# Optimization experiments

Measured on AMD Instinct MI355X. Metric: run time of the kernel, lower is better.

Reference implementation:

```python
import jax, jax.numpy as jnp
import numpy as np

B, T, C, H = 2, 2048, 2048, 16
HS = C // H
EPS = 1e-5


def _ln(x, w, b):
    mu = jnp.mean(x, axis=-1, keepdims=True)
    var = jnp.mean(jnp.square(x - mu), axis=-1, keepdims=True)
    return (x - mu) * jax.lax.rsqrt(var + EPS) * w + b


def setup_inputs() -> dict:
    key = jax.random.key(0)
    ks = jax.random.split(key, 8)
    s = 0.02
    return {
        "x": jax.random.normal(ks[0], (B, T, C), jnp.float32),
        "ln1_w": jnp.ones((C,), jnp.float32),
        "ln1_b": jnp.zeros((C,), jnp.float32),
        "w_qkv": jax.random.normal(ks[1], (C, 3 * C), jnp.float32) * s,
        "b_qkv": jnp.zeros((3 * C,), jnp.float32),
        "w_proj": jax.random.normal(ks[2], (C, C), jnp.float32) * s,
        "b_proj": jnp.zeros((C,), jnp.float32),
        "ln2_w": jnp.ones((C,), jnp.float32),
        "ln2_b": jnp.zeros((C,), jnp.float32),
        "w_fc": jax.random.normal(ks[3], (C, 4 * C), jnp.float32) * s,
        "b_fc": jnp.zeros((4 * C,), jnp.float32),
        "w_fc2": jax.random.normal(ks[4], (4 * C, C), jnp.float32) * s,
        "b_fc2": jnp.zeros((C,), jnp.float32),
    }


def reference(x, ln1_w, ln1_b, w_qkv, b_qkv, w_proj, b_proj,
              ln2_w, ln2_b, w_fc, b_fc, w_fc2, b_fc2):
    # --- attention branch (kv_cache=None -> L=0, burst=False, no padding mask) ---
    h = _ln(x, ln1_w, ln1_b)
    qkv = h @ w_qkv + b_qkv  # (B, T, 3C)
    q, k, v = jnp.split(qkv, 3, axis=-1)
    q = q.reshape(B, T, H, HS).transpose(0, 2, 1, 3)  # (B, H, T, HS)
    k = k.reshape(B, T, H, HS).transpose(0, 2, 1, 3)
    v = v.reshape(B, T, H, HS).transpose(0, 2, 1, 3)
    att = jnp.einsum('bhqd,bhkd->bhqk', q, k) * (1.0 / np.sqrt(HS))
    causal = jnp.tril(jnp.ones((T, T), bool))  # bias[0:T, 0:T]
    att = jnp.where(causal, att, -jnp.inf)
    att = jax.nn.softmax(att, axis=-1)
    y = jnp.einsum('bhqk,bhkd->bhqd', att, v)
    y = y.transpose(0, 2, 1, 3).reshape(B, T, C)
    y = y @ w_proj + b_proj
    x = x + y
    # --- MLP branch ---
    h = _ln(x, ln2_w, ln2_b)
    h = jax.nn.gelu(h @ w_fc + b_fc, approximate=False)
    x = x + (h @ w_fc2 + b_fc2)
    return x
```

## Files before the change

kernel.cpp:

```cpp
#include <hip/hip_runtime.h>
#include <hip/hip_bf16.h>
#include <cstdint>
#include <cstddef>

typedef __attribute__((ext_vector_type(8))) short bf16x8;
typedef __attribute__((ext_vector_type(4))) float f32x4;

#define DEVI __device__ __forceinline__

DEVI unsigned short f2bf(float f) {
  union { float f; unsigned u; } x; x.f = f;
  unsigned r = x.u + 0x7fffu + ((x.u >> 16) & 1u);
  return (unsigned short)(r >> 16);
}

DEVI float exp2fast(float x) {
#if __has_builtin(__builtin_amdgcn_exp2f)
  return __builtin_amdgcn_exp2f(x);
#else
  return exp2f(x);
#endif
}

DEVI void gload_lds16(const void* g, void* l) {
  __builtin_amdgcn_global_load_lds((const __attribute__((address_space(1))) void*)g,
                                   (__attribute__((address_space(3))) void*)l, 16, 0, 0);
}

DEVI f32x4 mfma16(bf16x8 a, bf16x8 b, f32x4 c) {
  return __builtin_amdgcn_mfma_f32_16x16x32_bf16(a, b, c, 0, 0, 0);
}

__global__ __launch_bounds__(256) void transpose_to_bf16(
    const float* __restrict__ w, unsigned short* __restrict__ wt, int K, int N) {
  __shared__ float tile[32][33];
  const int n0 = blockIdx.x * 32, k0 = blockIdx.y * 32;
  const int tx = threadIdx.x, ty = threadIdx.y;
#pragma unroll
  for (int i = 0; i < 4; i++)
    tile[ty + i * 8][tx] = w[(size_t)(k0 + ty + i * 8) * N + n0 + tx];
  __syncthreads();
#pragma unroll
  for (int i = 0; i < 4; i++)
    wt[(size_t)(n0 + ty + i * 8) * K + k0 + tx] = f2bf(tile[tx][ty + i * 8]);
}

__global__ __launch_bounds__(256) void transpose_v(
    const unsigned short* __restrict__ in, unsigned short* __restrict__ out) {
  __shared__ unsigned short tile[32][33];
  const int bh = blockIdx.z;
  const unsigned short* inp = in + (size_t)bh * 2048 * 128;
  unsigned short* op = out + (size_t)bh * 2048 * 128;
  const int t0 = blockIdx.x * 32, d0 = blockIdx.y * 32;
  const int tx = threadIdx.x, ty = threadIdx.y;
#pragma unroll
  for (int i = 0; i < 4; i++)
    tile[ty + i * 8][tx] = inp[(size_t)(t0 + ty + i * 8) * 128 + d0 + tx];
  __syncthreads();
#pragma unroll
  for (int i = 0; i < 4; i++)
    op[(size_t)(d0 + ty + i * 8) * 2048 + t0 + tx] = tile[tx][ty + i * 8];
}

__global__ __launch_bounds__(256) void ln_kernel(
    const float* __restrict__ x, const float* __restrict__ gw,
    const float* __restrict__ gb, unsigned short* __restrict__ out) {
  __shared__ float red[8];
  const int row = blockIdx.x, tid = threadIdx.x;
  const float* xr = x + (size_t)row * 2048;
  f32x4 a = *((const f32x4*)xr + tid * 2);
  f32x4 b = *((const f32x4*)xr + tid * 2 + 1);
  float s = a[0] + a[1] + a[2] + a[3] + b[0] + b[1] + b[2] + b[3];
#pragma unroll
  for (int m = 32; m >= 1; m >>= 1) s += __shfl_xor(s, m, 64);
  if ((tid & 63) == 0) red[tid >> 6] = s;
  __syncthreads();
  const float mu = (red[0] + red[1] + red[2] + red[3]) * (1.f / 2048.f);
  float d[8]; float ss = 0.f;
#pragma unroll
  for (int j = 0; j < 8; j++) {
    float v = ((j < 4) ? a[j] : b[j - 4]) - mu;
    d[j] = v; ss += v * v;
  }
#pragma unroll
  for (int m = 32; m >= 1; m >>= 1) ss += __shfl_xor(ss, m, 64);
  __syncthreads();
  if ((tid & 63) == 0) red[4 + (tid >> 6)] = ss;
  __syncthreads();
  const float var = (red[4] + red[5] + red[6] + red[7]) * (1.f / 2048.f);
  const float rstd = rsqrtf(var + 1e-5f);
  f32x4 w0 = *((const f32x4*)gw + tid * 2), w1 = *((const f32x4*)gw + tid * 2 + 1);
  f32x4 b0 = *((const f32x4*)gb + tid * 2), b1 = *((const f32x4*)gb + tid * 2 + 1);
  union { bf16x8 v; unsigned short u[8]; } o;
#pragma unroll
  for (int j = 0; j < 8; j++) {
    float wv = (j < 4) ? w0[j] : w1[j - 4];
    float bv = (j < 4) ? b0[j] : b1[j - 4];
    o.u[j] = f2bf(d[j] * rstd * wv + bv);
  }
  *(bf16x8*)(out + (size_t)row * 2048 + tid * 8) = o.v;
}

template <int EPI>
DEVI void epilogue_store(float v, int row, int col, int Nn,
                         const float* __restrict__ res, float* __restrict__ outf,
                         unsigned short* __restrict__ outb, unsigned short* __restrict__ oq,
                         unsigned short* __restrict__ ok, unsigned short* __restrict__ ov) {
  if constexpr (EPI == 0) {
    const int which = col >> 11, cc = col & 2047;
    const int hh = cc >> 7, hs = cc & 127;
    const int bb = row >> 11, tt = row & 2047;
    const size_t bh = (size_t)(bb * 16 + hh);
    const unsigned short bits = f2bf(v);
    if (which == 0) oq[(bh * 2048 + tt) * 128 + hs] = bits;
    else if (which == 1) ok[(bh * 2048 + tt) * 128 + hs] = bits;
    else ov[(bh * 2048 + tt) * 128 + hs] = bits;
  } else if constexpr (EPI == 1) {
    const float ge = 0.5f * v * (1.0f + erff(v * 0.70710678118654752f));
    outb[(size_t)row * Nn + col] = f2bf(ge);
  } else {
    outf[(size_t)row * Nn + col] = v + res[(size_t)row * Nn + col];
  }
}

template <int EPI>
__global__ __launch_bounds__(512, 2) void gemm256(
    const unsigned short* __restrict__ A, const unsigned short* __restrict__ Bt,
    const float* __restrict__ bias, const float* __restrict__ res,
    float* __restrict__ outf, unsigned short* __restrict__ outb,
    unsigned short* __restrict__ oq, unsigned short* __restrict__ ok,
    unsigned short* __restrict__ ov, int Nn, int Kk, int nbn) {
  __shared__ unsigned short As[2][256 * 64];
  __shared__ unsigned short Bs[2][256 * 64];
  const int tid = threadIdx.x;
  const int lane = tid & 63, wid = tid >> 6;
  const int i = lane & 15, g = lane >> 4;
  const int wm = wid >> 2, wn = wid & 3;
  const int nwg = gridDim.x;
  const int sid = (blockIdx.x & 7) * (nwg >> 3) + (blockIdx.x >> 3);
  const int m0 = (sid / nbn) * 256, n0 = (sid % nbn) * 256;

  auto stageA = [&](int bf, int kt, int h) {
#pragma unroll
    for (int c = 0; c < 2; c++) {
      const int cb = h * 1024 + c * 512 + wid * 64;
      const int ci = cb + lane;
      const int row = ci >> 3;
      const int kc = (ci & 7) ^ (row & 7);
      gload_lds16(A + (size_t)(m0 + row) * Kk + kt + kc * 8, &As[bf][(size_t)cb * 8]);
    }
  };
  auto stageB = [&](int bf, int kt, int h) {
#pragma unroll
    for (int c = 0; c < 2; c++) {
      const int cb = h * 1024 + c * 512 + wid * 64;
      const int ci = cb + lane;
      const int row = ci >> 3;
      const int kc = (ci & 7) ^ (row & 7);
      gload_lds16(Bt + (size_t)(n0 + row) * Kk + kt + kc * 8, &Bs[bf][(size_t)cb * 8]);
    }
  };
  auto ldA = [&](int bf, int jj, int ks) -> bf16x8 {
    const int row = (2 * jj + wm) * 16 + i;
    return *(const bf16x8*)((const char*)&As[bf][0] + row * 128 + ((((ks << 2) + g) ^ (i & 7)) << 4));
  };
  auto ldB = [&](int bf, int n, int ks) -> bf16x8 {
    const int row = (4 * n + wn) * 16 + i;
    return *(const bf16x8*)((const char*)&Bs[bf][0] + row * 128 + ((((ks << 2) + g) ^ (i & 7)) << 4));
  };

  f32x4 acc[8][4] = {};
  const int NT = Kk >> 6;

  stageA(0, 0, 0);
  stageB(0, 0, 0);
  stageB(0, 0, 1);
  stageA(0, 0, 1);
  asm volatile("s_waitcnt vmcnt(4)" ::: "memory");
  __builtin_amdgcn_s_barrier();
  __builtin_amdgcn_sched_barrier(0);

  bf16x8 a_lo[4][2], a_hi[4][2], b_lo[2][2], b_hi[2][2];
  for (int t = 0; t < NT; ++t) {
    const int cur = t & 1, nxt = cur ^ 1;
    const int ktn = (t + 1) << 6;
    const bool hn = (t + 1) < NT;
#pragma unroll
    for (int n = 0; n < 2; n++) { b_lo[n][0] = ldB(cur, n, 0); b_lo[n][1] = ldB(cur, n, 1); }
#pragma unroll
    for (int jj = 0; jj < 4; jj++) { a_lo[jj][0] = ldA(cur, jj, 0); a_lo[jj][1] = ldA(cur, jj, 1); }
    if (hn) stageA(nxt, ktn, 0);
    if (hn) asm volatile("s_waitcnt vmcnt(4)" ::: "memory");
    else    asm volatile("s_waitcnt vmcnt(2)" ::: "memory");
    __builtin_amdgcn_s_barrier();
    __builtin_amdgcn_sched_barrier(0);
    __builtin_amdgcn_s_setprio(1);
#pragma unroll
    for (int jj = 0; jj < 4; jj++)
#pragma unroll
      for (int n = 0; n < 2; n++) {
        acc[jj][n] = mfma16(a_lo[jj][0], b_lo[n][0], acc[jj][n]);
        acc[jj][n] = mfma16(a_lo[jj][1], b_lo[n][1], acc[jj][n]);
      }
    __builtin_amdgcn_s_setprio(0);
#pragma unroll
    for (int n = 0; n < 2; n++) { b_hi[n][0] = ldB(cur, 2 + n, 0); b_hi[n][1] = ldB(cur, 2 + n, 1); }
    if (hn) stageB(nxt, ktn, 0);
    if (hn) asm volatile("s_waitcnt vmcnt(4)" ::: "memory");
    else    asm volatile("s_waitcnt vmcnt(0)" ::: "memory");
    __builtin_amdgcn_s_barrier();
    __builtin_amdgcn_sched_barrier(0);
    __builtin_amdgcn_s_setprio(1);
#pragma unroll
    for (int jj = 0; jj < 4; jj++)
#pragma unroll
      for (int n = 0; n < 2; n++) {
        acc[jj][2 + n] = mfma16(a_lo[jj][0], b_hi[n][0], acc[jj][2 + n]);
        acc[jj][2 + n] = mfma16(a_lo[jj][1], b_hi[n][1], acc[jj][2 + n]);
      }
    __builtin_amdgcn_s_setprio(0);
#pragma unroll
    for (int jj = 0; jj < 4; jj++) { a_hi[jj][0] = ldA(cur, 4 + jj, 0); a_hi[jj][1] = ldA(cur, 4 + jj, 1); }
    if (hn) stageB(nxt, ktn, 1);
    __builtin_amdgcn_s_barrier();
    __builtin_amdgcn_sched_barrier(0);
    __builtin_amdgcn_s_setprio(1);
#pragma unroll
    for (int jj = 0; jj < 4; jj++)
#pragma unroll
      for (int n = 0; n < 2; n++) {
        acc[4 + jj][n] = mfma16(a_hi[jj][0], b_lo[n][0], acc[4 + jj][n]);
        acc[4 + jj][n] = mfma16(a_hi[jj][1], b_lo[n][1], acc[4 + jj][n]);
      }
    __builtin_amdgcn_s_setprio(0);
    if (hn) stageA(nxt, ktn, 1);
    if (hn) asm volatile("s_waitcnt vmcnt(4)" ::: "memory");
    __builtin_amdgcn_s_barrier();
    __builtin_amdgcn_sched_barrier(0);
    __builtin_amdgcn_s_setprio(1);
#pragma unroll
    for (int jj = 0; jj < 4; jj++)
#pragma unroll
      for (int n = 0; n < 2; n++) {
        acc[4 + jj][2 + n] = mfma16(a_hi[jj][0], b_hi[n][0], acc[4 + jj][2 + n]);
        acc[4 + jj][2 + n] = mfma16(a_hi[jj][1], b_hi[n][1], acc[4 + jj][2 + n]);
      }
    __builtin_amdgcn_s_setprio(0);
  }

#pragma unroll
  for (int jj = 0; jj < 8; jj++)
#pragma unroll
    for (int n = 0; n < 4; n++) {
      const int col = n0 + (4 * n + wn) * 16 + i;
      const float bv = bias[col];
#pragma unroll
      for (int r = 0; r < 4; r++) {
        const int row = m0 + (2 * jj + wm) * 16 + g * 4 + r;
        epilogue_store<EPI>(acc[jj][n][r] + bv, row, col, Nn, res, outf, outb, oq, ok, ov);
      }
    }
}

template <int EPI>
__global__ __launch_bounds__(512, 2) void gemm128(
    const unsigned short* __restrict__ A, const unsigned short* __restrict__ Bt,
    const float* __restrict__ bias, const float* __restrict__ res,
    float* __restrict__ outf, unsigned short* __restrict__ outb,
    unsigned short* __restrict__ oq, unsigned short* __restrict__ ok,
    unsigned short* __restrict__ ov, int Nn, int Kk, int nbn) {
  __shared__ unsigned short As[2][128 * 64];
  __shared__ unsigned short Bs[2][256 * 64];
  const int tid = threadIdx.x;
  const int lane = tid & 63, wid = tid >> 6;
  const int i = lane & 15, g = lane >> 4;
  const int wm = wid >> 2, wn = wid & 3;
  const int nwg = gridDim.x;
  const int sid = (blockIdx.x & 7) * (nwg >> 3) + (blockIdx.x >> 3);
  const int m0 = (sid / nbn) * 128, n0 = (sid % nbn) * 256;

  auto stageA = [&](int bf, int kt) {
#pragma unroll
    for (int c = 0; c < 2; c++) {
      const int cb = c * 512 + wid * 64;
      const int ci = cb + lane;
      const int row = ci >> 3;
      const int kc = (ci & 7) ^ (row & 7);
      gload_lds16(A + (size_t)(m0 + row) * Kk + kt + kc * 8, &As[bf][(size_t)cb * 8]);
    }
  };
  auto stageB = [&](int bf, int kt, int h) {
#pragma unroll
    for (int c = 0; c < 2; c++) {
      const int cb = h * 1024 + c * 512 + wid * 64;
      const int ci = cb + lane;
      const int row = ci >> 3;
      const int kc = (ci & 7) ^ (row & 7);
      gload_lds16(Bt + (size_t)(n0 + row) * Kk + kt + kc * 8, &Bs[bf][(size_t)cb * 8]);
    }
  };
  auto ldA = [&](int bf, int jj, int ks) -> bf16x8 {
    const int row = (2 * jj + wm) * 16 + i;
    return *(const bf16x8*)((const char*)&As[bf][0] + row * 128 + ((((ks << 2) + g) ^ (i & 7)) << 4));
  };
  auto ldB = [&](int bf, int n, int ks) -> bf16x8 {
    const int row = (4 * n + wn) * 16 + i;
    return *(const bf16x8*)((const char*)&Bs[bf][0] + row * 128 + ((((ks << 2) + g) ^ (i & 7)) << 4));
  };

  f32x4 acc[4][4] = {};
  const int NT = Kk >> 6;

  stageA(0, 0);
  stageB(0, 0, 0);
  stageB(0, 0, 1);
  asm volatile("s_waitcnt vmcnt(2)" ::: "memory");
  __builtin_amdgcn_s_barrier();
  __builtin_amdgcn_sched_barrier(0);

  bf16x8 af[4][2], b_lo[2][2], b_hi[2][2];
  for (int t = 0; t < NT; ++t) {
    const int cur = t & 1, nxt = cur ^ 1;
    const int ktn = (t + 1) << 6;
    const bool hn = (t + 1) < NT;
#pragma unroll
    for (int n = 0; n < 2; n++) { b_lo[n][0] = ldB(cur, n, 0); b_lo[n][1] = ldB(cur, n, 1); }
#pragma unroll
    for (int jj = 0; jj < 4; jj++) { af[jj][0] = ldA(cur, jj, 0); af[jj][1] = ldA(cur, jj, 1); }
    if (hn) { stageA(nxt, ktn); stageB(nxt, ktn, 0); }
    if (hn) asm volatile("s_waitcnt vmcnt(4)" ::: "memory");
    else    asm volatile("s_waitcnt vmcnt(0)" ::: "memory");
    __builtin_amdgcn_s_barrier();
    __builtin_amdgcn_sched_barrier(0);
    __builtin_amdgcn_s_setprio(1);
#pragma unroll
    for (int jj = 0; jj < 4; jj++)
#pragma unroll
      for (int n = 0; n < 2; n++) {
        acc[jj][n] = mfma16(af[jj][0], b_lo[n][0], acc[jj][n]);
        acc[jj][n] = mfma16(af[jj][1], b_lo[n][1], acc[jj][n]);
      }
    __builtin_amdgcn_s_setprio(0);
#pragma unroll
    for (int n = 0; n < 2; n++) { b_hi[n][0] = ldB(cur, 2 + n, 0); b_hi[n][1] = ldB(cur, 2 + n, 1); }
    if (hn) stageB(nxt, ktn, 1);
    if (hn) asm volatile("s_waitcnt vmcnt(2)" ::: "memory");
    __builtin_amdgcn_s_barrier();
    __builtin_amdgcn_sched_barrier(0);
    __builtin_amdgcn_s_setprio(1);
#pragma unroll
    for (int jj = 0; jj < 4; jj++)
#pragma unroll
      for (int n = 0; n < 2; n++) {
        acc[jj][2 + n] = mfma16(af[jj][0], b_hi[n][0], acc[jj][2 + n]);
        acc[jj][2 + n] = mfma16(af[jj][1], b_hi[n][1], acc[jj][2 + n]);
      }
    __builtin_amdgcn_s_setprio(0);
  }

#pragma unroll
  for (int jj = 0; jj < 4; jj++)
#pragma unroll
    for (int n = 0; n < 4; n++) {
      const int col = n0 + (4 * n + wn) * 16 + i;
      const float bv = bias[col];
#pragma unroll
      for (int r = 0; r < 4; r++) {
        const int row = m0 + (2 * jj + wm) * 16 + g * 4 + r;
        epilogue_store<EPI>(acc[jj][n][r] + bv, row, col, Nn, res, outf, outb, oq, ok, ov);
      }
    }
}

__global__ __launch_bounds__(256) void attn_kernel(
    const unsigned short* __restrict__ q, const unsigned short* __restrict__ k,
    const unsigned short* __restrict__ vt, unsigned short* __restrict__ y) {
  __shared__ unsigned short Ks[64 * 128];
  __shared__ unsigned short Vs[128 * 64];
  __shared__ unsigned short Ps[4][16 * 64];
  const int tid = threadIdx.x, lane = tid & 63, w = tid >> 6;
  const int i = lane & 15, g = lane >> 4;
  const int p = blockIdx.x, bh = blockIdx.y;
  const int q0A = p * 64, q0B = (31 - p) * 64;
  const int tB = 31 - p;
  const size_t hb = (size_t)bh * (2048 * 128);
  const float sc2 = 0.08838834764831845f * 1.44269504088896341f;

  bf16x8 qfA[4], qfB[4];
  {
    const int qra = q0A + w * 16 + i, qrb = q0B + w * 16 + i;
#pragma unroll
    for (int kc = 0; kc < 4; kc++) {
      qfA[kc] = *(const bf16x8*)(q + hb + (size_t)qra * 128 + kc * 32 + g * 8);
      qfB[kc] = *(const bf16x8*)(q + hb + (size_t)qrb * 128 + kc * 32 + g * 8);
    }
  }
  f32x4 oA[8] = {}, oB[8] = {};
  float mA = -__builtin_inff(), lA = 0.f, mB = -__builtin_inff(), lB = 0.f;

  auto proc = [&](const bf16x8 (&qf)[4], f32x4 (&oacc)[8], float& mrun, float& lrun,
                  bool diag) {
    f32x4 st[4];
#pragma unroll
    for (int ct = 0; ct < 4; ct++) {
      f32x4 a = {};
      const int kvr = ct * 16 + i;
#pragma unroll
      for (int kc = 0; kc < 4; kc++) {
        bf16x8 kf = *(const bf16x8*)((char*)Ks + kvr * 256 + (((kc * 4 + g) ^ (i & 7)) << 4));
        a = mfma16(kf, qf[kc], a);
      }
      st[ct] = a;
    }
    float tm = -__builtin_inff();
    const int ql = w * 16 + i;
#pragma unroll
    for (int ct = 0; ct < 4; ct++)
#pragma unroll
      for (int r = 0; r < 4; r++) {
        float v = st[ct][r] * sc2;
        if (diag) {
          const int kvl = ct * 16 + g * 4 + r;
          if (kvl > ql) v = -__builtin_inff();
        }
        st[ct][r] = v;
        tm = fmaxf(tm, v);
      }
    tm = fmaxf(tm, __shfl_xor(tm, 16, 64));
    tm = fmaxf(tm, __shfl_xor(tm, 32, 64));
    if (!__all(tm - mrun <= 8.f)) {
      const float mnew = fmaxf(mrun, tm);
      const float al = exp2fast(mrun - mnew);
      float ar[4];
#pragma unroll
      for (int r = 0; r < 4; r++) ar[r] = __shfl(al, g * 4 + r, 64);
#pragma unroll
      for (int dt = 0; dt < 8; dt++)
#pragma unroll
        for (int r = 0; r < 4; r++) oacc[dt][r] *= ar[r];
      lrun *= al;
      mrun = mnew;
    }
    float ps = 0.f;
#pragma unroll
    for (int ct = 0; ct < 4; ct++)
#pragma unroll
      for (int r = 0; r < 4; r++) {
        const float pv = exp2fast(st[ct][r] - mrun);
        st[ct][r] = pv;
        ps += pv;
      }
    ps += __shfl_xor(ps, 16, 64);
    ps += __shfl_xor(ps, 32, 64);
    lrun += ps;
#pragma unroll
    for (int ct = 0; ct < 4; ct++) {
      unsigned w0, w1;
      asm("v_cvt_pk_bf16_f32 %0, %1, %2" : "=v"(w0) : "v"(st[ct][0]), "v"(st[ct][1]));
      asm("v_cvt_pk_bf16_f32 %0, %1, %2" : "=v"(w1) : "v"(st[ct][2]), "v"(st[ct][3]));
      char* pb = (char*)&Ps[w][0] + i * 128 +
                 ((((2 * ct + (g >> 1)) ^ (i & 7)) << 4) + (g & 1) * 8);
      *(uint2*)pb = make_uint2(w0, w1);
    }
    bf16x8 pf[2];
#pragma unroll
    for (int kvc = 0; kvc < 2; kvc++)
      pf[kvc] = *(const bf16x8*)((char*)&Ps[w][0] + i * 128 + (((kvc * 4 + g) ^ (i & 7)) << 4));
#pragma unroll
    for (int dt = 0; dt < 8; dt++) {
      const int dr = dt * 16 + i;
#pragma unroll
      for (int kvc = 0; kvc < 2; kvc++) {
        bf16x8 vf = *(const bf16x8*)((char*)Vs + dr * 128 + (((kvc * 4 + g) ^ (dr & 7)) << 4));
        oacc[dt] = mfma16(pf[kvc], vf, oacc[dt]);
      }
    }
  };

  for (int t = 0; t <= tB; ++t) {
    const int j0 = t * 64;
    __syncthreads();
#pragma unroll
    for (int it = 0; it < 4; it++) {
      const int ci = it * 256 + tid;
      const int kv = ci >> 4, ccl = ci & 15;
      gload_lds16(k + hb + (size_t)(j0 + kv) * 128 + ((ccl ^ (kv & 7)) << 3),
                  (char*)Ks + (size_t)(it * 256 + w * 64) * 16);
      const int dd = ci >> 3, c2l = ci & 7;
      gload_lds16(vt + hb + (size_t)dd * 2048 + j0 + ((c2l ^ (dd & 7)) << 3),
                  (char*)Vs + (size_t)(it * 256 + w * 64) * 16);
    }
    __syncthreads();
    if (t <= p) proc(qfA, oA, mA, lA, t == p);
    proc(qfB, oB, mB, lB, t == tB);
  }

  const int bb = bh >> 4, hh = bh & 15;
  auto finish = [&](const f32x4 (&oacc)[8], float lrun, int q0s) {
    const float inv_i = 1.f / lrun;
    float ir[4];
#pragma unroll
    for (int r = 0; r < 4; r++) ir[r] = __shfl(inv_i, g * 4 + r, 64);
#pragma unroll
    for (int r = 0; r < 4; r++) {
      const int row = q0s + w * 16 + g * 4 + r;
#pragma unroll
      for (int dt = 0; dt < 8; dt++) {
        const int d = dt * 16 + i;
        y[((size_t)(bb * 2048 + row)) * 2048 + hh * 128 + d] = f2bf(oacc[dt][r] * ir[r]);
      }
    }
  };
  finish(oA, lA, q0A);
  finish(oB, lB, q0B);
}

extern "C" void kernel_launch(void* const* d_in, const int* in_sizes, int n_in,
                              void* d_out, int out_size, void* d_ws, size_t ws_size,
                              hipStream_t stream) {
  const float* x      = (const float*)d_in[0];
  const float* ln1_w  = (const float*)d_in[1];
  const float* ln1_b  = (const float*)d_in[2];
  const float* w_qkv  = (const float*)d_in[3];
  const float* b_qkv  = (const float*)d_in[4];
  const float* w_proj = (const float*)d_in[5];
  const float* b_proj = (const float*)d_in[6];
  const float* ln2_w  = (const float*)d_in[7];
  const float* ln2_b  = (const float*)d_in[8];
  const float* w_fc   = (const float*)d_in[9];
  const float* b_fc   = (const float*)d_in[10];
  const float* w_fc2  = (const float*)d_in[11];
  const float* b_fc2  = (const float*)d_in[12];

  char* ws = (char*)d_ws;
  unsigned short* wt_qkv  = (unsigned short*)(ws + 0);
  unsigned short* wt_proj = (unsigned short*)(ws + 25165824);
  unsigned short* qb      = (unsigned short*)(ws + 33554432);
  unsigned short* kb      = (unsigned short*)(ws + 50331648);
  unsigned short* wt_fc   = (unsigned short*)(ws + 67108864);
  unsigned short* wt_fc2  = (unsigned short*)(ws + 100663296);
  unsigned short* hb      = (unsigned short*)(ws + 134217728);
  unsigned short* vtb     = (unsigned short*)(ws + 150994944);
  unsigned short* yb      = (unsigned short*)(ws + 167772160);
  float*          x1      = (float*)(ws + 184549376);
  unsigned short* hfc     = (unsigned short*)(ws + 0);
  float* outp = (float*)d_out;

  dim3 tb(32, 8);
  transpose_to_bf16<<<dim3(6144 / 32, 2048 / 32), tb, 0, stream>>>(w_qkv, wt_qkv, 2048, 6144);
  transpose_to_bf16<<<dim3(2048 / 32, 2048 / 32), tb, 0, stream>>>(w_proj, wt_proj, 2048, 2048);
  transpose_to_bf16<<<dim3(8192 / 32, 2048 / 32), tb, 0, stream>>>(w_fc, wt_fc, 2048, 8192);
  transpose_to_bf16<<<dim3(2048 / 32, 8192 / 32), tb, 0, stream>>>(w_fc2, wt_fc2, 8192, 2048);

  ln_kernel<<<4096, 256, 0, stream>>>(x, ln1_w, ln1_b, hb);

  gemm128<0><<<768, 512, 0, stream>>>(
      hb, wt_qkv, b_qkv, nullptr, nullptr, nullptr, qb, kb, yb, 6144, 2048, 24);
  transpose_v<<<dim3(2048 / 32, 128 / 32, 32), tb, 0, stream>>>(yb, vtb);

  attn_kernel<<<dim3(16, 32), 256, 0, stream>>>(qb, kb, vtb, yb);

  gemm128<2><<<256, 512, 0, stream>>>(
      yb, wt_proj, b_proj, x, x1, nullptr, nullptr, nullptr, nullptr, 2048, 2048, 8);

  ln_kernel<<<4096, 256, 0, stream>>>(x1, ln2_w, ln2_b, hb);

  gemm256<1><<<512, 512, 0, stream>>>(
      hb, wt_fc, b_fc, nullptr, nullptr, hfc, nullptr, nullptr, nullptr, 8192, 2048, 32);

  gemm128<2><<<256, 512, 0, stream>>>(
      hfc, wt_fc2, b_fc2, x1, outp, nullptr, nullptr, nullptr, nullptr, 2048, 8192, 8);
}
```

Measured before the change: 664.7 us.

## Software-pipeline GEMM main loops: prefetch next tile fragments and stage two tiles ahead

Restructures both GEMM kernels' K-loops so LDS fragment reads for the next iteration and global-to-LDS staging for tile t+2 are issued between MFMA phases. Previously the first fragment loads of each iteration sat on the critical path after the barrier. This is meant to hide LDS and global latency behind MFMA work. The trade-off is more complex vmcnt and barrier bookkeeping, with a risk of races on the double buffer and higher register pressure.

New measurement: 695.3 us. 1.05x slower.

```diff
diff --git a/kernel.cpp b/kernel.cpp
--- a/kernel.cpp
+++ b/kernel.cpp
@@ -176,24 +176,27 @@
   stageB(0, 0, 0);
   stageB(0, 0, 1);
   stageA(0, 0, 1);
-  asm volatile("s_waitcnt vmcnt(4)" ::: "memory");
+  if (NT > 1) stageB(1, 64, 0);
+  asm volatile("s_waitcnt vmcnt(6)" ::: "memory");
   __builtin_amdgcn_s_barrier();
   __builtin_amdgcn_sched_barrier(0);
 
   bf16x8 a_lo[4][2], a_hi[4][2], b_lo[2][2], b_hi[2][2];
+#pragma unroll
+  for (int n = 0; n < 2; n++) { b_lo[n][0] = ldB(0, n, 0); b_lo[n][1] = ldB(0, n, 1); }
+#pragma unroll
+  for (int jj = 0; jj < 4; jj++) { a_lo[jj][0] = ldA(0, jj, 0); a_lo[jj][1] = ldA(0, jj, 1); }
+  asm volatile("s_waitcnt vmcnt(4)" ::: "memory");
+
   for (int t = 0; t < NT; ++t) {
     const int cur = t & 1, nxt = cur ^ 1;
-    const int ktn = (t + 1) << 6;
-    const bool hn = (t + 1) < NT;
-#pragma unroll
-    for (int n = 0; n < 2; n++) { b_lo[n][0] = ldB(cur, n, 0); b_lo[n][1] = ldB(cur, n, 1); }
-#pragma unroll
-    for (int jj = 0; jj < 4; jj++) { a_lo[jj][0] = ldA(cur, jj, 0); a_lo[jj][1] = ldA(cur, jj, 1); }
-    if (hn) stageA(nxt, ktn, 0);
-    if (hn) asm volatile("s_waitcnt vmcnt(4)" ::: "memory");
-    else    asm volatile("s_waitcnt vmcnt(2)" ::: "memory");
+    const int ktn = (t + 1) << 6, ktn2 = (t + 2) << 6;
+    const bool hn = (t + 1) < NT, hn2 = (t + 2) < NT;
     __builtin_amdgcn_s_barrier();
     __builtin_amdgcn_sched_barrier(0);
+#pragma unroll
+    for (int n = 0; n < 2; n++) { b_hi[n][0] = ldB(cur, 2 + n, 0); b_hi[n][1] = ldB(cur, 2 + n, 1); }
+    if (hn) stageA(nxt, ktn, 0);
     __builtin_amdgcn_s_setprio(1);
 #pragma unroll
     for (int jj = 0; jj < 4; jj++)
@@ -203,13 +206,13 @@
         acc[jj][n] = mfma16(a_lo[jj][1], b_lo[n][1], acc[jj][n]);
       }
     __builtin_amdgcn_s_setprio(0);
-#pragma unroll
-    for (int n = 0; n < 2; n++) { b_hi[n][0] = ldB(cur, 2 + n, 0); b_hi[n][1] = ldB(cur, 2 + n, 1); }
-    if (hn) stageB(nxt, ktn, 0);
     if (hn) asm volatile("s_waitcnt vmcnt(4)" ::: "memory");
     else    asm volatile("s_waitcnt vmcnt(0)" ::: "memory");
     __builtin_amdgcn_s_barrier();
     __builtin_amdgcn_sched_barrier(0);
+#pragma unroll
+    for (int jj = 0; jj < 4; jj++) { a_hi[jj][0] = ldA(cur, 4 + jj, 0); a_hi[jj][1] = ldA(cur, 4 + jj, 1); }
+    if (hn) stageB(nxt, ktn, 1);
     __builtin_amdgcn_s_setprio(1);
 #pragma unroll
     for (int jj = 0; jj < 4; jj++)
@@ -219,21 +222,6 @@
         acc[jj][2 + n] = mfma16(a_lo[jj][1], b_hi[n][1], acc[jj][2 + n]);
       }
     __builtin_amdgcn_s_setprio(0);
-#pragma unroll
-    for (int jj = 0; jj < 4; jj++) { a_hi[jj][0] = ldA(cur, 4 + jj, 0); a_hi[jj][1] = ldA(cur, 4 + jj, 1); }
-    if (hn) stageB(nxt, ktn, 1);
-    __builtin_amdgcn_s_barrier();
-    __builtin_amdgcn_sched_barrier(0);
-    __builtin_amdgcn_s_setprio(1);
-#pragma unroll
-    for (int jj = 0; jj < 4; jj++)
-#pragma unroll
-      for (int n = 0; n < 2; n++) {
-        acc[4 + jj][n] = mfma16(a_hi[jj][0], b_lo[n][0], acc[4 + jj][n]);
-        acc[4 + jj][n] = mfma16(a_hi[jj][1], b_lo[n][1], acc[4 + jj][n]);
-      }
-    __builtin_amdgcn_s_setprio(0);
-    if (hn) stageA(nxt, ktn, 1);
     if (hn) asm volatile("s_waitcnt vmcnt(4)" ::: "memory");
     __builtin_amdgcn_s_barrier();
     __builtin_amdgcn_sched_barrier(0);
@@ -242,10 +230,34 @@
     for (int jj = 0; jj < 4; jj++)
 #pragma unroll
       for (int n = 0; n < 2; n++) {
+        acc[4 + jj][n] = mfma16(a_hi[jj][0], b_lo[n][0], acc[4 + jj][n]);
+        acc[4 + jj][n] = mfma16(a_hi[jj][1], b_lo[n][1], acc[4 + jj][n]);
+      }
+    __builtin_amdgcn_s_setprio(0);
+    if (hn) {
+#pragma unroll
+      for (int n = 0; n < 2; n++) { b_lo[n][0] = ldB(nxt, n, 0); b_lo[n][1] = ldB(nxt, n, 1); }
+      stageA(nxt, ktn, 1);
+      asm volatile("s_waitcnt vmcnt(4)" ::: "memory");
+    }
+    __builtin_amdgcn_s_barrier();
+    __builtin_amdgcn_sched_barrier(0);
+    if (hn) {
+#pragma unroll
+      for (int jj = 0; jj < 4; jj++) { a_lo[jj][0] = ldA(nxt, jj, 0); a_lo[jj][1] = ldA(nxt, jj, 1); }
+    }
+    if (hn2) stageB(cur, ktn2, 0);
+    __builtin_amdgcn_s_setprio(1);
+#pragma unroll
+    for (int jj = 0; jj < 4; jj++)
+#pragma unroll
+      for (int n = 0; n < 2; n++) {
         acc[4 + jj][2 + n] = mfma16(a_hi[jj][0], b_hi[n][0], acc[4 + jj][2 + n]);
         acc[4 + jj][2 + n] = mfma16(a_hi[jj][1], b_hi[n][1], acc[4 + jj][2 + n]);
       }
     __builtin_amdgcn_s_setprio(0);
+    if (hn2)      asm volatile("s_waitcnt vmcnt(4)" ::: "memory");
+    else if (hn)  asm volatile("s_waitcnt vmcnt(2)" ::: "memory");
   }
 
 #pragma unroll
@@ -314,24 +326,27 @@
   stageA(0, 0);
   stageB(0, 0, 0);
   stageB(0, 0, 1);
-  asm volatile("s_waitcnt vmcnt(2)" ::: "memory");
+  if (NT > 1) { stageA(1, 64); stageB(1, 64, 0); }
+  asm volatile("s_waitcnt vmcnt(6)" ::: "memory");
   __builtin_amdgcn_s_barrier();
   __builtin_amdgcn_sched_barrier(0);
 
   bf16x8 af[4][2], b_lo[2][2], b_hi[2][2];
+#pragma unroll
+  for (int n = 0; n < 2; n++) { b_lo[n][0] = ldB(0, n, 0); b_lo[n][1] = ldB(0, n, 1); }
+#pragma unroll
+  for (int jj = 0; jj < 4; jj++) { af[jj][0] = ldA(0, jj, 0); af[jj][1] = ldA(0, jj, 1); }
+  asm volatile("s_waitcnt vmcnt(4)" ::: "memory");
+
   for (int t = 0; t < NT; ++t) {
     const int cur = t & 1, nxt = cur ^ 1;
-    const int ktn = (t + 1) << 6;
-    const bool hn = (t + 1) < NT;
-#pragma unroll
-    for (int n = 0; n < 2; n++) { b_lo[n][0] = ldB(cur, n, 0); b_lo[n][1] = ldB(cur, n, 1); }
-#pragma unroll
-    for (int jj = 0; jj < 4; jj++) { af[jj][0] = ldA(cur, jj, 0); af[jj][1] = ldA(cur, jj, 1); }
-    if (hn) { stageA(nxt, ktn); stageB(nxt, ktn, 0); }
-    if (hn) asm volatile("s_waitcnt vmcnt(4)" ::: "memory");
-    else    asm volatile("s_waitcnt vmcnt(0)" ::: "memory");
+    const int ktn = (t + 1) << 6, ktn2 = (t + 2) << 6;
+    const bool hn = (t + 1) < NT, hn2 = (t + 2) < NT;
     __builtin_amdgcn_s_barrier();
     __builtin_amdgcn_sched_barrier(0);
+#pragma unroll
+    for (int n = 0; n < 2; n++) { b_hi[n][0] = ldB(cur, 2 + n, 0); b_hi[n][1] = ldB(cur, 2 + n, 1); }
+    if (hn) stageB(nxt, ktn, 1);
     __builtin_amdgcn_s_setprio(1);
 #pragma unroll
     for (int jj = 0; jj < 4; jj++)
@@ -341,12 +356,13 @@
         acc[jj][n] = mfma16(af[jj][1], b_lo[n][1], acc[jj][n]);
       }
     __builtin_amdgcn_s_setprio(0);
-#pragma unroll
-    for (int n = 0; n < 2; n++) { b_hi[n][0] = ldB(cur, 2 + n, 0); b_hi[n][1] = ldB(cur, 2 + n, 1); }
-    if (hn) stageB(nxt, ktn, 1);
     if (hn) asm volatile("s_waitcnt vmcnt(2)" ::: "memory");
     __builtin_amdgcn_s_barrier();
     __builtin_amdgcn_sched_barrier(0);
+    if (hn) {
+#pragma unroll
+      for (int n = 0; n < 2; n++) { b_lo[n][0] = ldB(nxt, n, 0); b_lo[n][1] = ldB(nxt, n, 1); }
+    }
     __builtin_amdgcn_s_setprio(1);
 #pragma unroll
     for (int jj = 0; jj < 4; jj++)
@@ -356,6 +372,16 @@
         acc[jj][2 + n] = mfma16(af[jj][1], b_hi[n][1], acc[jj][2 + n]);
       }
     __builtin_amdgcn_s_setprio(0);
+    if (hn) {
+#pragma unroll
+      for (int jj = 0; jj < 4; jj++) { af[jj][0] = ldA(nxt, jj, 0); af[jj][1] = ldA(nxt, jj, 1); }
+    }
+    if (hn2) {
+      stageA(cur, ktn2); stageB(cur, ktn2, 0);
+      asm volatile("s_waitcnt vmcnt(4)" ::: "memory");
+    } else if (hn) {
+      asm volatile("s_waitcnt vmcnt(0)" ::: "memory");
+    }
   }
 
 #pragma unroll
```
